# Kernel tuning notes

Hardware: AMD Instinct MI355X
Metric: run time of the kernel (lower is better)

The kernel has to match this reference:

```python
import jax, jax.numpy as jnp
import numpy as np

NT, NS, NH = 1096, 2048, 16

def setup_inputs() -> dict:
    key = jax.random.key(0)
    ks = jax.random.split(key, 6)
    # precipitation (non-negative) and temperature (can be +/-)
    P = jax.random.uniform(ks[0], (NT, NS), dtype=jnp.float32) * 10.0
    T = jax.random.normal(ks[1], (NT, NS), dtype=jnp.float32) * 10.0
    w_i = jax.random.uniform(ks[2], (NH,), minval=-1.0, maxval=1.0, dtype=jnp.float32)
    w_o = jax.random.uniform(ks[3], (NH,), minval=-1.0, maxval=1.0, dtype=jnp.float32)
    w_l = jax.random.uniform(ks[4], (NH,), minval=-1.0, maxval=1.0, dtype=jnp.float32)  # LinearBucket.w
    w_s = jax.random.uniform(ks[5], (NH,), minval=-1.0, maxval=2.0, dtype=jnp.float32)  # SnowBucket.w
    return dict(P=P, T=T, w_i=w_i, w_o=w_o, w_l=w_l, w_s=w_s)


def reference(P, T, w_i, w_o, w_l, w_s):
    # Time-invariant gate factors (Dropout is identity in eval mode)
    melt_coef = jnp.exp(w_s) + 1.0          # [nh]
    gi = jax.nn.sigmoid(w_i)                # [nh] input gate
    gl = jax.nn.sigmoid(w_l)                # [nh] linear-bucket release fraction
    a = jax.nn.softmax(w_o)                 # [nh] output mixing weights

    ns = P.shape[1]
    nh = w_i.shape[0]
    s0 = jnp.zeros((ns, nh), P.dtype)
    h0 = jnp.zeros((ns, nh), P.dtype)

    def step(carry, pt):
        s, h = carry
        Pk, Tk = pt                          # [ns]
        # SnowBucket (nm=0: melt m = min(potential melt, snow store))
        sm = jax.nn.relu(Tk)[:, None] * melt_coef      # [ns, nh]
        m = jnp.minimum(sm, s)
        sn = s - m + jnp.where(Tk < 0, Pk, 0.0)[:, None]
        x = jnp.where(Tk > 0, Pk, 0.0)[:, None] + m
        # input gate + LinearBucket
        xin = x * gi
        q = (xin + h) * gl
        hn = h - q + xin
        Qk = jnp.sum(q * a, axis=1)                    # [ns]
        return (sn, hn), (Qk, hn, sn)

    _, (Q, H, S) = jax.lax.scan(step, (s0, h0), (P, T))
    return Q, H, S
```

## Files before the change

kernel.cpp:

```cpp
#include <hip/hip_runtime.h>


constexpr int NT  = 1096;
constexpr int NS  = 2048;
constexpr int NH  = 16;
constexpr int NSH = NS * NH;
constexpr int SG  = 8;
constexpr int NC  = 16;
constexpr int LA  = 69;
constexpr int LB  = 68;
constexpr int BT  = 1024;
constexpr int NXCD = 8;
constexpr int RES = SG * NH;

__device__ __forceinline__ float sigm(float x) { return 1.0f / (1.0f + expf(-x)); }

__global__ __launch_bounds__(BT, 1) void waternet_fused(
    const float* __restrict__ P, const float* __restrict__ T,
    const float* __restrict__ w_i, const float* __restrict__ w_o,
    const float* __restrict__ w_l, const float* __restrict__ w_s,
    float* __restrict__ Q, float* __restrict__ H, float* __restrict__ S)
{
    __shared__ float2 PTs[SG][NT + 2];
    __shared__ float bufA[BT * 2];
    __shared__ float bufB[BT * 2];
    __shared__ float bufC[BT * 2];

    const int nwg  = NS / SG;
    const int cpx  = nwg / NXCD;
    const int bid  = (int)blockIdx.x;
    const int lbid = (bid % NXCD) * cpx + bid / NXCD;

    const int tid  = (int)threadIdx.x;
    const int hh2  = tid & 7;
    const int sl   = (tid >> 3) & (SG - 1);
    const int c    = tid >> 6;
    const int site0 = lbid * SG;

    const int t0  = (c < 8) ? (LA * c) : (LA * 8 + LB * (c - 8));
    const int len = (c < 8) ? LA : LB;

    for (int e = tid; e < SG * NT; e += BT) {
        const int t  = e >> 3;
        const int s2 = e & 7;
        const float p  = P[(size_t)t * NS + site0 + s2];
        const float tt = T[(size_t)t * NS + site0 + s2];
        PTs[s2][t] = make_float2(p, tt);
    }

    float mc[2], gi[2], gl[2], cl[2];
    #pragma unroll
    for (int p = 0; p < 2; ++p) {
        const int hh = hh2 * 2 + p;
        mc[p] = expf(w_s[hh]) + 1.0f;
        gi[p] = sigm(w_i[hh]);
        gl[p] = sigm(w_l[hh]);
        cl[p] = 1.0f - gl[p];
    }

    __syncthreads();

    float A[2] = {0.0f, 0.0f}, B[2] = {-1e38f, -1e38f};
    {
        const float2* pts = &PTs[sl][t0];
        auto stepAB = [&](float2 pt) {
            const float tpos = fmaxf(pt.y, 0.0f);
            const float pnn  = (pt.y < 0.0f) ? pt.x : 0.0f;
            #pragma unroll
            for (int p = 0; p < 2; ++p) {
                const float at = pnn - tpos * mc[p];
                A[p] += at;
                B[p] = fmaxf(B[p] + at, pnn);
            }
        };
        int i = 0;
        for (; i + 4 <= len; i += 4) {
            float2 v0 = pts[i], v1 = pts[i+1], v2 = pts[i+2], v3 = pts[i+3];
            stepAB(v0); stepAB(v1); stepAB(v2); stepAB(v3);
        }
        for (; i < len; ++i) stepAB(pts[i]);
    }
    bufA[tid * 2]     = A[0];
    bufA[tid * 2 + 1] = A[1];
    bufB[tid * 2]     = B[0];
    bufB[tid * 2 + 1] = B[1];
    __syncthreads();

    if (tid < RES) {
        float s = 0.0f;
        #pragma unroll
        for (int k = 0; k < NC; ++k) {
            const int idx = k * RES + tid;
            bufC[idx] = s;
            s = fmaxf(s + bufA[idx], bufB[idx]);
        }
    }
    __syncthreads();

    float s[2], hp[2] = {0.0f, 0.0f};
    s[0] = bufC[tid * 2];
    s[1] = bufC[tid * 2 + 1];
    {
        const float2* pts = &PTs[sl][t0];
        float2* Sp = (float2*)(S + (size_t)t0 * NSH + (size_t)site0 * NH
                               + sl * NH + hh2 * 2);
        auto step2 = [&](float2 pt, int i) {
            const float tpos = fmaxf(pt.y, 0.0f);
            const float pnn  = (pt.y < 0.0f) ? pt.x : 0.0f;
            const float ppp  = (pt.y > 0.0f) ? pt.x : 0.0f;
            float2 sv;
            #pragma unroll
            for (int p = 0; p < 2; ++p) {
                const float m = fminf(tpos * mc[p], s[p]);
                s[p] = s[p] - m + pnn;
                const float xin = (ppp + m) * gi[p];
                hp[p] = cl[p] * (hp[p] + xin);
                (p ? sv.y : sv.x) = s[p];
            }
            Sp[(size_t)i * (NSH / 2)] = sv;
        };
        int i = 0;
        for (; i + 4 <= len; i += 4) {
            float2 v0 = pts[i], v1 = pts[i+1], v2 = pts[i+2], v3 = pts[i+3];
            step2(v0, i); step2(v1, i+1); step2(v2, i+2); step2(v3, i+3);
        }
        for (; i < len; ++i) step2(pts[i], i);
    }
    bufA[tid * 2]     = hp[0];
    bufA[tid * 2 + 1] = hp[1];
    __syncthreads();

    if (tid < RES) {
        const float clr = 1.0f - sigm(w_l[tid & (NH - 1)]);
        const float pA = powf(clr, (float)LA);
        const float pB = powf(clr, (float)LB);
        float h = 0.0f;
        #pragma unroll
        for (int k = 0; k < NC; ++k) {
            const int idx = k * RES + tid;
            bufB[idx] = h;
            h = ((k < 8) ? pA : pB) * h + bufA[idx];
        }
    }
    __syncthreads();

    float aw[2];
    {
        float mx = -1e30f;
        #pragma unroll
        for (int j = 0; j < NH; ++j) mx = fmaxf(mx, w_o[j]);
        float den = 0.0f;
        #pragma unroll
        for (int j = 0; j < NH; ++j) den += expf(w_o[j] - mx);
        aw[0] = expf(w_o[hh2 * 2]     - mx) / den;
        aw[1] = expf(w_o[hh2 * 2 + 1] - mx) / den;
    }

    s[0] = bufC[tid * 2];
    s[1] = bufC[tid * 2 + 1];
    float h[2];
    h[0] = bufB[tid * 2];
    h[1] = bufB[tid * 2 + 1];
    {
        const float2* pts = &PTs[sl][t0];
        float2* Hp = (float2*)(H + (size_t)t0 * NSH + (size_t)site0 * NH
                               + sl * NH + hh2 * 2);
        float* Qp = Q + (size_t)t0 * NS + site0 + sl;
        auto step3 = [&](float2 pt, int i) {
            const float tpos = fmaxf(pt.y, 0.0f);
            const float pnn  = (pt.y < 0.0f) ? pt.x : 0.0f;
            const float ppp  = (pt.y > 0.0f) ? pt.x : 0.0f;
            float2 hv;
            float qa = 0.0f;
            #pragma unroll
            for (int p = 0; p < 2; ++p) {
                const float m = fminf(tpos * mc[p], s[p]);
                s[p] = s[p] - m + pnn;
                const float xin = (ppp + m) * gi[p];
                const float q   = (xin + h[p]) * gl[p];
                h[p] = cl[p] * (h[p] + xin);
                (p ? hv.y : hv.x) = h[p];
                qa += q * aw[p];
            }
            Hp[(size_t)i * (NSH / 2)] = hv;
            qa += __shfl_xor(qa, 1, 8);
            qa += __shfl_xor(qa, 2, 8);
            qa += __shfl_xor(qa, 4, 8);
            if (hh2 == 0) Qp[(size_t)i * NS] = qa;
        };
        int i = 0;
        for (; i + 4 <= len; i += 4) {
            float2 v0 = pts[i], v1 = pts[i+1], v2 = pts[i+2], v3 = pts[i+3];
            step3(v0, i); step3(v1, i+1); step3(v2, i+2); step3(v3, i+3);
        }
        for (; i < len; ++i) step3(pts[i], i);
    }
}

extern "C" void kernel_launch(void* const* d_in, const int* in_sizes, int n_in,
                              void* d_out, int out_size, void* d_ws, size_t ws_size,
                              hipStream_t stream) {
    const float* P   = (const float*)d_in[0];
    const float* T   = (const float*)d_in[1];
    const float* w_i = (const float*)d_in[2];
    const float* w_o = (const float*)d_in[3];
    const float* w_l = (const float*)d_in[4];
    const float* w_s = (const float*)d_in[5];

    float* Q = (float*)d_out;
    float* H = Q + (size_t)NT * NS;
    float* S = H + (size_t)NT * NS * NH;

    waternet_fused<<<NS / SG, BT, 0, stream>>>(P, T, w_i, w_o, w_l, w_s, Q, H, S);
}
```

Baseline: 315.3 us.

## Give each thread four hidden units and split time into 32 chunks

Each thread now owns four hidden units instead of two, so a site's 16 units take 4 lanes and the time axis splits into 32 chunks of about 34 steps instead of 16 chunks of about 68. Writes of S and H become float4 stores, the Q reduction needs only two shuffles, and the P/T staging uses float4 global loads. This halves the serial chunk length per thread and widens stores, at the cost of a longer serial cross-chunk scan over 32 chunks, more registers per thread and 4-way scattered LDS stores during staging.

Measured after the change: 312.1 us. No clear change (-1.0%).

```diff
diff --git a/kernel.cpp b/kernel.cpp
--- a/kernel.cpp
+++ b/kernel.cpp
@@ -6,9 +6,9 @@
 constexpr int NH  = 16;
 constexpr int NSH = NS * NH;
 constexpr int SG  = 8;
-constexpr int NC  = 16;
-constexpr int LA  = 69;
-constexpr int LB  = 68;
+constexpr int NC  = 32;
+constexpr int LA  = 35;
+constexpr int LB  = 34;
 constexpr int BT  = 1024;
 constexpr int NXCD = 8;
 constexpr int RES = SG * NH;
@@ -22,9 +22,9 @@
     float* __restrict__ Q, float* __restrict__ H, float* __restrict__ S)
 {
     __shared__ float2 PTs[SG][NT + 2];
-    __shared__ float bufA[BT * 2];
-    __shared__ float bufB[BT * 2];
-    __shared__ float bufC[BT * 2];
+    __shared__ float bufA[NC * RES];
+    __shared__ float bufB[NC * RES];
+    __shared__ float bufC[NC * RES];
 
     const int nwg  = NS / SG;
     const int cpx  = nwg / NXCD;
@@ -32,26 +32,29 @@
     const int lbid = (bid % NXCD) * cpx + bid / NXCD;
 
     const int tid  = (int)threadIdx.x;
-    const int hh2  = tid & 7;
-    const int sl   = (tid >> 3) & (SG - 1);
-    const int c    = tid >> 6;
+    const int q    = tid & 3;
+    const int sl   = (tid >> 2) & (SG - 1);
+    const int c    = tid >> 5;
     const int site0 = lbid * SG;
 
     const int t0  = (c < 8) ? (LA * c) : (LA * 8 + LB * (c - 8));
     const int len = (c < 8) ? LA : LB;
 
-    for (int e = tid; e < SG * NT; e += BT) {
-        const int t  = e >> 3;
-        const int s2 = e & 7;
-        const float p  = P[(size_t)t * NS + site0 + s2];
-        const float tt = T[(size_t)t * NS + site0 + s2];
-        PTs[s2][t] = make_float2(p, tt);
-    }
-
-    float mc[2], gi[2], gl[2], cl[2];
-    #pragma unroll
-    for (int p = 0; p < 2; ++p) {
-        const int hh = hh2 * 2 + p;
+    for (int e = tid; e < 2 * NT; e += BT) {
+        const int t  = e >> 1;
+        const int hf = (e & 1) * 4;
+        const float4 p4 = *(const float4*)(P + (size_t)t * NS + site0 + hf);
+        const float4 t4 = *(const float4*)(T + (size_t)t * NS + site0 + hf);
+        PTs[hf + 0][t] = make_float2(p4.x, t4.x);
+        PTs[hf + 1][t] = make_float2(p4.y, t4.y);
+        PTs[hf + 2][t] = make_float2(p4.z, t4.z);
+        PTs[hf + 3][t] = make_float2(p4.w, t4.w);
+    }
+
+    float mc[4], gi[4], gl[4], cl[4];
+    #pragma unroll
+    for (int p = 0; p < 4; ++p) {
+        const int hh = q * 4 + p;
         mc[p] = expf(w_s[hh]) + 1.0f;
         gi[p] = sigm(w_i[hh]);
         gl[p] = sigm(w_l[hh]);
@@ -60,14 +63,15 @@
 
     __syncthreads();
 
-    float A[2] = {0.0f, 0.0f}, B[2] = {-1e38f, -1e38f};
+    float A[4] = {0.0f, 0.0f, 0.0f, 0.0f};
+    float B[4] = {-1e38f, -1e38f, -1e38f, -1e38f};
     {
         const float2* pts = &PTs[sl][t0];
         auto stepAB = [&](float2 pt) {
             const float tpos = fmaxf(pt.y, 0.0f);
             const float pnn  = (pt.y < 0.0f) ? pt.x : 0.0f;
             #pragma unroll
-            for (int p = 0; p < 2; ++p) {
+            for (int p = 0; p < 4; ++p) {
                 const float at = pnn - tpos * mc[p];
                 A[p] += at;
                 B[p] = fmaxf(B[p] + at, pnn);
@@ -80,10 +84,11 @@
         }
         for (; i < len; ++i) stepAB(pts[i]);
     }
-    bufA[tid * 2]     = A[0];
-    bufA[tid * 2 + 1] = A[1];
-    bufB[tid * 2]     = B[0];
-    bufB[tid * 2 + 1] = B[1];
+    #pragma unroll
+    for (int p = 0; p < 4; ++p) {
+        bufA[tid * 4 + p] = A[p];
+        bufB[tid * 4 + p] = B[p];
+    }
     __syncthreads();
 
     if (tid < RES) {
@@ -97,27 +102,27 @@
     }
     __syncthreads();
 
-    float s[2], hp[2] = {0.0f, 0.0f};
-    s[0] = bufC[tid * 2];
-    s[1] = bufC[tid * 2 + 1];
+    float s[4], hp[4] = {0.0f, 0.0f, 0.0f, 0.0f};
+    #pragma unroll
+    for (int p = 0; p < 4; ++p) s[p] = bufC[tid * 4 + p];
     {
         const float2* pts = &PTs[sl][t0];
-        float2* Sp = (float2*)(S + (size_t)t0 * NSH + (size_t)site0 * NH
-                               + sl * NH + hh2 * 2);
+        float4* Sp = (float4*)(S + (size_t)t0 * NSH + (size_t)site0 * NH
+                               + sl * NH + q * 4);
         auto step2 = [&](float2 pt, int i) {
             const float tpos = fmaxf(pt.y, 0.0f);
             const float pnn  = (pt.y < 0.0f) ? pt.x : 0.0f;
             const float ppp  = (pt.y > 0.0f) ? pt.x : 0.0f;
-            float2 sv;
+            float4 sv;
             #pragma unroll
-            for (int p = 0; p < 2; ++p) {
+            for (int p = 0; p < 4; ++p) {
                 const float m = fminf(tpos * mc[p], s[p]);
                 s[p] = s[p] - m + pnn;
                 const float xin = (ppp + m) * gi[p];
                 hp[p] = cl[p] * (hp[p] + xin);
-                (p ? sv.y : sv.x) = s[p];
+                ((float*)&sv)[p] = s[p];
             }
-            Sp[(size_t)i * (NSH / 2)] = sv;
+            Sp[(size_t)i * (NSH / 4)] = sv;
         };
         int i = 0;
         for (; i + 4 <= len; i += 4) {
@@ -126,8 +131,8 @@
         }
         for (; i < len; ++i) step2(pts[i], i);
     }
-    bufA[tid * 2]     = hp[0];
-    bufA[tid * 2 + 1] = hp[1];
+    #pragma unroll
+    for (int p = 0; p < 4; ++p) bufA[tid * 4 + p] = hp[p];
     __syncthreads();
 
     if (tid < RES) {
@@ -144,7 +149,7 @@
     }
     __syncthreads();
 
-    float aw[2];
+    float aw[4];
     {
         float mx = -1e30f;
         #pragma unroll
@@ -152,41 +157,41 @@
         float den = 0.0f;
         #pragma unroll
         for (int j = 0; j < NH; ++j) den += expf(w_o[j] - mx);
-        aw[0] = expf(w_o[hh2 * 2]     - mx) / den;
-        aw[1] = expf(w_o[hh2 * 2 + 1] - mx) / den;
-    }
-
-    s[0] = bufC[tid * 2];
-    s[1] = bufC[tid * 2 + 1];
-    float h[2];
-    h[0] = bufB[tid * 2];
-    h[1] = bufB[tid * 2 + 1];
+        #pragma unroll
+        for (int p = 0; p < 4; ++p) aw[p] = expf(w_o[q * 4 + p] - mx) / den;
+    }
+
+    float h[4];
+    #pragma unroll
+    for (int p = 0; p < 4; ++p) {
+        s[p] = bufC[tid * 4 + p];
+        h[p] = bufB[tid * 4 + p];
+    }
     {
         const float2* pts = &PTs[sl][t0];
-        float2* Hp = (float2*)(H + (size_t)t0 * NSH + (size_t)site0 * NH
-                               + sl * NH + hh2 * 2);
+        float4* Hp = (float4*)(H + (size_t)t0 * NSH + (size_t)site0 * NH
+                               + sl * NH + q * 4);
         float* Qp = Q + (size_t)t0 * NS + site0 + sl;
         auto step3 = [&](float2 pt, int i) {
             const float tpos = fmaxf(pt.y, 0.0f);
             const float pnn  = (pt.y < 0.0f) ? pt.x : 0.0f;
             const float ppp  = (pt.y > 0.0f) ? pt.x : 0.0f;
-            float2 hv;
+            float4 hv;
             float qa = 0.0f;
             #pragma unroll
-            for (int p = 0; p < 2; ++p) {
+            for (int p = 0; p < 4; ++p) {
                 const float m = fminf(tpos * mc[p], s[p]);
                 s[p] = s[p] - m + pnn;
                 const float xin = (ppp + m) * gi[p];
-                const float q   = (xin + h[p]) * gl[p];
+                const float qq  = (xin + h[p]) * gl[p];
                 h[p] = cl[p] * (h[p] + xin);
-                (p ? hv.y : hv.x) = h[p];
-                qa += q * aw[p];
+                ((float*)&hv)[p] = h[p];
+                qa += qq * aw[p];
             }
-            Hp[(size_t)i * (NSH / 2)] = hv;
-            qa += __shfl_xor(qa, 1, 8);
-            qa += __shfl_xor(qa, 2, 8);
-            qa += __shfl_xor(qa, 4, 8);
-            if (hh2 == 0) Qp[(size_t)i * NS] = qa;
+            Hp[(size_t)i * (NSH / 4)] = hv;
+            qa += __shfl_xor(qa, 1, 4);
+            qa += __shfl_xor(qa, 2, 4);
+            if (q == 0) Qp[(size_t)i * NS] = qa;
         };
         int i = 0;
         for (; i + 4 <= len; i += 4) {
```
